# Optimization experiments

Hardware: AMD Instinct MI355X
Metric: run time of the kernel (lower is better)

Reference implementation:

```python
import jax, jax.numpy as jnp
import numpy as np

DIM = 768
NUM_HEADS = 12
HEAD_DIM = DIM // NUM_HEADS
SCALE = HEAD_DIM ** -0.5


def setup_inputs() -> dict:
    key = jax.random.key(0)
    k1, k2, k3, k4 = jax.random.split(key, 4)
    B, N = 4, 2048
    x = jax.random.normal(k1, (B, N, DIM), dtype=jnp.float32)
    w_qkv = jax.random.normal(k2, (DIM, 3 * DIM), dtype=jnp.float32) * (DIM ** -0.5)
    w_proj = jax.random.normal(k3, (DIM, DIM), dtype=jnp.float32) * (DIM ** -0.5)
    b_proj = jax.random.normal(k4, (DIM,), dtype=jnp.float32) * 0.02
    return {"x": x, "w_qkv": w_qkv, "w_proj": w_proj, "b_proj": b_proj}


def reference(x, w_qkv, w_proj, b_proj):
    B, N, C = x.shape
    H, Dh = NUM_HEADS, HEAD_DIM
    # qkv: [B, N, 3, H, Dh] -> q,k,v each [B, H, N, Dh]
    qkv = (x @ w_qkv).reshape(B, N, 3, H, Dh)
    q = qkv[:, :, 0].transpose(0, 2, 1, 3) * SCALE
    k = qkv[:, :, 1].transpose(0, 2, 1, 3)
    v = qkv[:, :, 2].transpose(0, 2, 1, 3)
    attn = jax.nn.softmax(jnp.einsum('bhnd,bhmd->bhnm', q, k), axis=-1)
    out = jnp.einsum('bhnm,bhmd->bhnd', attn, v)  # [B, H, N, Dh]
    out = out.transpose(0, 2, 1, 3).reshape(B, N, C)
    return out @ w_proj + b_proj
```

## Files before the change

kernel.cpp:

```cpp
#include <hip/hip_runtime.h>

typedef unsigned short u16;
typedef __bf16 bf16x8 __attribute__((ext_vector_type(8)));
typedef __bf16 bf16x4 __attribute__((ext_vector_type(4)));
typedef short s16x4 __attribute__((ext_vector_type(4)));
typedef float f32x4 __attribute__((ext_vector_type(4)));
typedef _Float16 f16x4 __attribute__((ext_vector_type(4)));
typedef unsigned short u16x8 __attribute__((ext_vector_type(8)));
typedef unsigned short u16x4 __attribute__((ext_vector_type(4)));

__device__ __forceinline__ u16 f2bf(float x) {
  union { float f; unsigned u; } c; c.f = x;
  unsigned r = c.u + 0x7FFFu + ((c.u >> 16) & 1u);
  return (u16)(r >> 16);
}

__device__ __forceinline__ void glds16(const void* g, void* s) {
  __builtin_amdgcn_global_load_lds(
      (const __attribute__((address_space(1))) unsigned int*)g,
      (__attribute__((address_space(3))) unsigned int*)s, 16, 0, 0);
}

__global__ __launch_bounds__(256) void k_pre(const float* __restrict__ x,
                                             u16* __restrict__ xbf,
                                             const float* __restrict__ wq,
                                             u16* __restrict__ wqt,
                                             const float* __restrict__ wp,
                                             u16* __restrict__ wpt) {
  __shared__ float tile[64 * 68];
  int bx = blockIdx.x;
  int tid = threadIdx.x;
  if (bx < 3072) {
    int i = bx * 256 + tid;
    const f32x4* xp = (const f32x4*)x + (size_t)i * 2;
    f32x4 a = xp[0], b = xp[1];
    u16x8 r;
    r[0] = f2bf(a[0]); r[1] = f2bf(a[1]); r[2] = f2bf(a[2]); r[3] = f2bf(a[3]);
    r[4] = f2bf(b[0]); r[5] = f2bf(b[1]); r[6] = f2bf(b[2]); r[7] = f2bf(b[3]);
    *((u16x8*)xbf + i) = r;
    return;
  }
  const float* src; u16* dst; int Nn, n0, k0;
  const int K = 768;
  if (bx < 3504) { int b2 = bx - 3072; src = wq; dst = wqt; Nn = 2304;
                   n0 = (b2 % 36) * 64; k0 = (b2 / 36) * 64; }
  else           { int b2 = bx - 3504; src = wp; dst = wpt; Nn = 768;
                   n0 = (b2 % 12) * 64; k0 = (b2 / 12) * 64; }
  int rr = tid >> 4, cc = tid & 15;
#pragma unroll
  for (int r = 0; r < 4; ++r) {
    int k = r * 16 + rr;
    f32x4 v = *(const f32x4*)(src + (size_t)(k0 + k) * Nn + n0 + cc * 4);
    *(f32x4*)(tile + k * 68 + cc * 4) = v;
  }
  __syncthreads();
#pragma unroll
  for (int r = 0; r < 4; ++r) {
    int n = r * 16 + rr;
    u16x4 o;
#pragma unroll
    for (int j = 0; j < 4; ++j) o[j] = f2bf(tile[(cc * 4 + j) * 68 + n]);
    *(u16x4*)(dst + (size_t)(n0 + n) * K + k0 + cc * 4) = o;
  }
}

template <int BM, int N, bool PROJ>
__global__ __launch_bounds__(256) void k_gemm(const u16* __restrict__ A,
                                              const u16* __restrict__ Bt,
                                              u16* __restrict__ Co,
                                              float* __restrict__ Cf,
                                              const float* __restrict__ bias,
                                              u16* __restrict__ vt) {
  const int K = 768;
  const int FI = BM / 32;
  __shared__ u16 lA[BM * 64];
  __shared__ u16 lB[128 * 64];
  const int tid = threadIdx.x;
  const int wave = tid >> 6, lane = tid & 63;
  const int lr = lane & 15, lq = lane >> 4;
  const int m0 = blockIdx.x * BM, n0 = blockIdx.y * 128;
  const int wr = (wave >> 1) * (BM / 2), wc = (wave & 1) * 64;
  f32x4 acc[FI][4] = {};
  for (int k0 = 0; k0 < K; k0 += 64) {
#pragma unroll
    for (int r = 0; r < BM / 32; ++r) {
      int ch = r * 256 + tid;
      int mm = ch >> 3, cs = ch & 7;
      glds16(A + (size_t)(m0 + mm) * K + k0 + ((cs ^ (mm & 7)) << 3), lA + ch * 8);
    }
#pragma unroll
    for (int r = 0; r < 4; ++r) {
      int ch = r * 256 + tid;
      int mm = ch >> 3, cs = ch & 7;
      glds16(Bt + (size_t)(n0 + mm) * K + k0 + ((cs ^ (mm & 7)) << 3), lB + ch * 8);
    }
    __syncthreads();
#pragma unroll
    for (int ks = 0; ks < 2; ++ks) {
      bf16x8 af[FI], bfr[4];
#pragma unroll
      for (int f = 0; f < FI; ++f) {
        int ma = wr + f * 16 + lr;
        af[f] = *(const bf16x8*)(lA + (ma * 8 + ((ks * 4 + lq) ^ (ma & 7))) * 8);
      }
#pragma unroll
      for (int f = 0; f < 4; ++f) {
        int nb = wc + f * 16 + lr;
        bfr[f] = *(const bf16x8*)(lB + (nb * 8 + ((ks * 4 + lq) ^ (nb & 7))) * 8);
      }
#pragma unroll
      for (int fi = 0; fi < FI; ++fi)
#pragma unroll
        for (int fj = 0; fj < 4; ++fj)
          acc[fi][fj] = __builtin_amdgcn_mfma_f32_16x16x32_bf16(
              af[fi], bfr[fj], acc[fi][fj], 0, 0, 0);
    }
    __syncthreads();
  }
#pragma unroll
  for (int fi = 0; fi < FI; ++fi) {
#pragma unroll
    for (int fj = 0; fj < 4; ++fj) {
      int row = m0 + wr + fi * 16 + lq * 4;
      int col = n0 + wc + fj * 16 + lr;
      if constexpr (PROJ) {
        float bv = bias[col];
#pragma unroll
        for (int g = 0; g < 4; ++g)
          Cf[(size_t)(row + g) * N + col] = acc[fi][fj][g] + bv;
      } else {
        if (n0 + wc >= 1536) {
          int hh = (col - 1536) >> 6, dd = col & 63;
          u16x4 o;
#pragma unroll
          for (int g = 0; g < 4; ++g) o[g] = f2bf(acc[fi][fj][g]);
          *(u16x4*)(vt + (((size_t)(row >> 11) * 12 + hh) * 64 + dd) * 2048 +
                    (row & 2047)) = o;
        } else {
          const float qs = 0.18033688011112042f;
          float s = (col < 768) ? qs : 1.0f;
#pragma unroll
          for (int g = 0; g < 4; ++g)
            Co[(size_t)(row + g) * N + col] = f2bf(acc[fi][fj][g] * s);
        }
      }
    }
  }
}

__global__ __launch_bounds__(256, 2) void k_attn(const u16* __restrict__ qkv,
                                                 const u16* __restrict__ vt,
                                                 u16* __restrict__ p0,
                                                 u16* __restrict__ p1,
                                                 float* __restrict__ Lp) {
  const int SEQ = 2048, C3 = 2304;
  __shared__ u16 lK[2][128 * 64];
  __shared__ u16 lV[2][64 * 128];
  const int tid = threadIdx.x;
  const int wave = tid >> 6, lane = tid & 63;
  const int lr = lane & 15, lq = lane >> 4;
  const int n0 = blockIdx.x * 128;
  const int bh = blockIdx.y;
  const int jh = blockIdx.z;
  const int b = bh / 12, h = bh % 12;
  const u16* qb = qkv + (size_t)b * SEQ * C3 + h * 64;
  const u16* kb = qb + 768;
  const u16* vb = vt + (size_t)bh * 64 * SEQ;

#pragma unroll
  for (int r = 0; r < 4; ++r) {
    int ch = r * 256 + tid;
    int mm = ch >> 3, cs = ch & 7;
    glds16(qb + (size_t)(n0 + mm) * C3 + ((cs ^ (mm & 7)) << 3), lK[0] + ch * 8);
  }
  __syncthreads();
  bf16x8 qf[2][2];
#pragma unroll
  for (int rf = 0; rf < 2; ++rf) {
    int mq = wave * 32 + rf * 16 + lr;
#pragma unroll
    for (int ks = 0; ks < 2; ++ks)
      qf[rf][ks] = *(const bf16x8*)(lK[0] + (mq * 8 + ((ks * 4 + lq) ^ (mq & 7))) * 8);
  }
  __syncthreads();

  const f32x4 biasC = {-8.f, -8.f, -8.f, -8.f};
  const s16x4 onesA = {16256, 16256, 16256, 16256};
  f32x4 O[2][4] = {};
  f32x4 L5[2] = {};

  const int smm = tid >> 3, scs = tid & 7;
  const int sdd = tid >> 4, sct = tid & 15;

  auto stage = [&](int t, int buf) {
    int j0 = jh * 1024 + t * 128;
#pragma unroll
    for (int r = 0; r < 4; ++r) {
      int ch = r * 256 + tid;
      int mm = (r << 5) + smm;
      glds16(kb + (size_t)(j0 + mm) * C3 + ((scs ^ (mm & 7)) << 3),
             lK[buf] + ch * 8);
      int dd = (r << 4) + sdd;
      glds16(vb + (size_t)dd * SEQ + j0 + ((sct ^ (dd & 7)) << 3),
             lV[buf] + ch * 8);
    }
  };

  stage(0, 0);
  for (int t = 0; t < 8; ++t) {
    const int cur = t & 1;
    const u16* K_ = lK[cur];
    const u16* V_ = lV[cur];
    asm volatile("s_barrier" ::: "memory");
    if (t < 7) {
      stage(t + 1, cur ^ 1);
      asm volatile("s_waitcnt vmcnt(8)" ::: "memory");
    } else {
      asm volatile("s_waitcnt vmcnt(0)" ::: "memory");
    }
    asm volatile("s_barrier" ::: "memory");

    f32x4 S[8][2];
#pragma unroll
    for (int cf = 0; cf < 8; ++cf) {
      int j = cf * 16 + lr;
      bf16x8 kf = *(const bf16x8*)(K_ + (j * 8 + (lq ^ (j & 7))) * 8);
#pragma unroll
      for (int rf = 0; rf < 2; ++rf)
        S[cf][rf] = __builtin_amdgcn_mfma_f32_16x16x32_bf16(
            kf, qf[rf][0], biasC, 0, 0, 0);
    }
#pragma unroll
    for (int cf = 0; cf < 8; ++cf) {
      int j = cf * 16 + lr;
      bf16x8 kf = *(const bf16x8*)(K_ + (j * 8 + ((4 + lq) ^ (j & 7))) * 8);
#pragma unroll
      for (int rf = 0; rf < 2; ++rf)
        S[cf][rf] = __builtin_amdgcn_mfma_f32_16x16x32_bf16(
            kf, qf[rf][1], S[cf][rf], 0, 0, 0);
    }
    union PU { bf16x4 b; s16x4 s; } P[8][2];
#pragma unroll
    for (int cf = 0; cf < 8; ++cf)
#pragma unroll
      for (int rf = 0; rf < 2; ++rf) {
        bf16x4 pb;
#pragma unroll
        for (int g = 0; g < 4; ++g)
          pb[g] = (__bf16)__builtin_amdgcn_exp2f(S[cf][rf][g]);
        P[cf][rf].b = pb;
      }
#pragma unroll
    for (int cf = 0; cf < 8; ++cf) {
      int c2 = cf * 2 + (lq >> 1);
#pragma unroll
      for (int rf = 0; rf < 2; ++rf)
        L5[rf] = __builtin_amdgcn_mfma_f32_16x16x16bf16_1k(
            onesA, P[cf][rf].s, L5[rf], 0, 0, 0);
#pragma unroll
      for (int df = 0; df < 4; ++df) {
        int d = df * 16 + lr;
        s16x4 vf = *(const s16x4*)(V_ + d * 128 + ((c2 ^ (d & 7)) << 3) + (lq & 1) * 4);
#pragma unroll
        for (int rf = 0; rf < 2; ++rf)
          O[rf][df] = __builtin_amdgcn_mfma_f32_16x16x16bf16_1k(
              vf, P[cf][rf].s, O[rf][df], 0, 0, 0);
      }
    }
  }

  u16* pd = jh ? p1 : p0;
  float* Lb = Lp + (size_t)(jh * 48 + bh) * 2048;
#pragma unroll
  for (int rf = 0; rf < 2; ++rf) {
    int rowl = n0 + wave * 32 + rf * 16 + lr;
    if (lq == 0) Lb[rowl] = L5[rf][0];
    size_t row = (size_t)b * SEQ + rowl;
#pragma unroll
    for (int df = 0; df < 4; ++df) {
      union { f16x4 h; u16x4 u; } o;
#pragma unroll
      for (int g = 0; g < 4; ++g) o.h[g] = (_Float16)O[rf][df][g];
      *(u16x4*)(pd + row * 768 + h * 64 + df * 16 + lq * 4) = o.u;
    }
  }
}

__global__ __launch_bounds__(256) void k_merge(const u16* __restrict__ p0,
                                               u16* __restrict__ p1,
                                               const float* __restrict__ Lp) {
  int t = blockIdx.x * 256 + threadIdx.x;
  int row = t / 192, c4 = (t % 192) * 4;
  int hh = c4 >> 6;
  int bh = (row >> 11) * 12 + hh, rowl = row & 2047;
  float l = Lp[(size_t)bh * 2048 + rowl] + Lp[(size_t)(48 + bh) * 2048 + rowl];
  float inv = 1.0f / l;
  size_t off = (size_t)row * 768 + c4;
  union { f16x4 h; u16x4 u; } a, bb;
  a.u = *(const u16x4*)(p0 + off);
  bb.u = *(const u16x4*)(p1 + off);
  u16x4 o;
#pragma unroll
  for (int g = 0; g < 4; ++g)
    o[g] = f2bf(((float)a.h[g] + (float)bb.h[g]) * inv);
  *(u16x4*)(p1 + off) = o;
}

extern "C" void kernel_launch(void* const* d_in, const int* in_sizes, int n_in,
                              void* d_out, int out_size, void* d_ws, size_t ws_size,
                              hipStream_t stream) {
  const float* x = (const float*)d_in[0];
  const float* w_qkv = (const float*)d_in[1];
  const float* w_proj = (const float*)d_in[2];
  const float* b_proj = (const float*)d_in[3];
  float* out = (float*)d_out;
  char* ws = (char*)d_ws;
  u16* x_bf    = (u16*)(ws);
  u16* wqkv_t  = (u16*)(ws + 12582912);
  u16* wproj_t = (u16*)(ws + 16121856);
  u16* qkv     = (u16*)(ws + 17301504);
  u16* vt      = (u16*)(ws + 55050240);
  u16* aout    = (u16*)(ws + 67633152);
  float* Lp    = (float*)wqkv_t;

  k_pre<<<3648, 256, 0, stream>>>(x, x_bf, w_qkv, wqkv_t, w_proj, wproj_t);
  k_gemm<128, 2304, false><<<dim3(64, 18), 256, 0, stream>>>(x_bf, wqkv_t, qkv,
                                                             nullptr, nullptr, vt);
  k_attn<<<dim3(16, 48, 2), 256, 0, stream>>>(qkv, vt, x_bf, aout, Lp);
  k_merge<<<6144, 256, 0, stream>>>(x_bf, aout, Lp);
  k_gemm<64, 768, true><<<dim3(128, 6), 256, 0, stream>>>(aout, wproj_t, nullptr,
                                                          out, b_proj, nullptr);
}
```

Baseline: 233.6 us.

## Widen attention query tile to 256 rows and use 16x16x32 MFMA for PV

Each attention block now handles 256 query rows (64 per wave) instead of 128, so every K/V tile staged into LDS is reused across twice as many queries and the grid shrinks by half. The PV product and the row-sum now use the 16x16x32 bf16 MFMA on 8-element P fragments rather than the 16x16x16 variant. To support this, the QKV GEMM writes V-transposed with a permuted sequence order so that each lane's 8-element V read lines up with the S fragment layout. This raises register pressure (4x4 accumulators plus 4x2 Q fragments) and halves the block count, which may hurt occupancy and load balance.

```diff
diff --git a/kernel.cpp b/kernel.cpp
--- a/kernel.cpp
+++ b/kernel.cpp
@@ -2,8 +2,6 @@
 
 typedef unsigned short u16;
 typedef __bf16 bf16x8 __attribute__((ext_vector_type(8)));
-typedef __bf16 bf16x4 __attribute__((ext_vector_type(4)));
-typedef short s16x4 __attribute__((ext_vector_type(4)));
 typedef float f32x4 __attribute__((ext_vector_type(4)));
 typedef _Float16 f16x4 __attribute__((ext_vector_type(4)));
 typedef unsigned short u16x8 __attribute__((ext_vector_type(8)));
@@ -131,11 +129,15 @@
       } else {
         if (n0 + wc >= 1536) {
           int hh = (col - 1536) >> 6, dd = col & 63;
+          int sl = row & 2047;
+          int g4 = (sl >> 2) & 31;
+          int p = ((g4 >> 3) << 3) | ((g4 & 3) << 1) | ((g4 >> 2) & 1);
+          int seqp = (sl & ~127) | (p << 2);
           u16x4 o;
 #pragma unroll
           for (int g = 0; g < 4; ++g) o[g] = f2bf(acc[fi][fj][g]);
           *(u16x4*)(vt + (((size_t)(row >> 11) * 12 + hh) * 64 + dd) * 2048 +
-                    (row & 2047)) = o;
+                    seqp) = o;
         } else {
           const float qs = 0.18033688011112042f;
           float s = (col < 768) ? qs : 1.0f;
@@ -154,12 +156,11 @@
                                                  u16* __restrict__ p1,
                                                  float* __restrict__ Lp) {
   const int SEQ = 2048, C3 = 2304;
-  __shared__ u16 lK[2][128 * 64];
-  __shared__ u16 lV[2][64 * 128];
+  __shared__ u16 lds[32768];
   const int tid = threadIdx.x;
   const int wave = tid >> 6, lane = tid & 63;
   const int lr = lane & 15, lq = lane >> 4;
-  const int n0 = blockIdx.x * 128;
+  const int n0 = blockIdx.x * 256;
   const int bh = blockIdx.y;
   const int jh = blockIdx.z;
   const int b = bh / 12, h = bh % 12;
@@ -168,49 +169,53 @@
   const u16* vb = vt + (size_t)bh * 64 * SEQ;
 
 #pragma unroll
-  for (int r = 0; r < 4; ++r) {
+  for (int r = 0; r < 8; ++r) {
     int ch = r * 256 + tid;
     int mm = ch >> 3, cs = ch & 7;
-    glds16(qb + (size_t)(n0 + mm) * C3 + ((cs ^ (mm & 7)) << 3), lK[0] + ch * 8);
+    glds16(qb + (size_t)(n0 + mm) * C3 + ((cs ^ (mm & 7)) << 3), lds + ch * 8);
   }
   __syncthreads();
-  bf16x8 qf[2][2];
-#pragma unroll
-  for (int rf = 0; rf < 2; ++rf) {
-    int mq = wave * 32 + rf * 16 + lr;
+  bf16x8 qf[4][2];
+#pragma unroll
+  for (int rf = 0; rf < 4; ++rf) {
+    int mq = wave * 64 + rf * 16 + lr;
 #pragma unroll
     for (int ks = 0; ks < 2; ++ks)
-      qf[rf][ks] = *(const bf16x8*)(lK[0] + (mq * 8 + ((ks * 4 + lq) ^ (mq & 7))) * 8);
+      qf[rf][ks] = *(const bf16x8*)(lds + (mq * 8 + ((ks * 4 + lq) ^ (mq & 7))) * 8);
   }
   __syncthreads();
 
   const f32x4 biasC = {-8.f, -8.f, -8.f, -8.f};
-  const s16x4 onesA = {16256, 16256, 16256, 16256};
-  f32x4 O[2][4] = {};
-  f32x4 L5[2] = {};
-
-  const int smm = tid >> 3, scs = tid & 7;
-  const int sdd = tid >> 4, sct = tid & 15;
+  union { u16x8 u; bf16x8 b; } onesU;
+#pragma unroll
+  for (int e = 0; e < 8; ++e) onesU.u[e] = 0x3F80;
+  const bf16x8 onesA = onesU.b;
+  f32x4 O[4][4] = {};
+  f32x4 L5[4] = {};
 
   auto stage = [&](int t, int buf) {
     int j0 = jh * 1024 + t * 128;
+    u16* K_ = lds + buf * 8192;
+    u16* V_ = lds + 16384 + buf * 8192;
 #pragma unroll
     for (int r = 0; r < 4; ++r) {
       int ch = r * 256 + tid;
-      int mm = (r << 5) + smm;
-      glds16(kb + (size_t)(j0 + mm) * C3 + ((scs ^ (mm & 7)) << 3),
-             lK[buf] + ch * 8);
-      int dd = (r << 4) + sdd;
-      glds16(vb + (size_t)dd * SEQ + j0 + ((sct ^ (dd & 7)) << 3),
-             lV[buf] + ch * 8);
+      int mm = ch >> 3, cs = ch & 7;
+      glds16(kb + (size_t)(j0 + mm) * C3 + ((cs ^ (mm & 7)) << 3), K_ + ch * 8);
+    }
+#pragma unroll
+    for (int r = 0; r < 4; ++r) {
+      int ch = r * 256 + tid;
+      int dd = ch >> 4, ct = ch & 15;
+      glds16(vb + (size_t)dd * SEQ + j0 + ((ct ^ (dd & 7)) << 3), V_ + ch * 8);
     }
   };
 
   stage(0, 0);
   for (int t = 0; t < 8; ++t) {
     const int cur = t & 1;
-    const u16* K_ = lK[cur];
-    const u16* V_ = lV[cur];
+    const u16* K_ = lds + cur * 8192;
+    const u16* V_ = lds + 16384 + cur * 8192;
     asm volatile("s_barrier" ::: "memory");
     if (t < 7) {
       stage(t + 1, cur ^ 1);
@@ -220,51 +225,48 @@
     }
     asm volatile("s_barrier" ::: "memory");
 
-    f32x4 S[8][2];
-#pragma unroll
-    for (int cf = 0; cf < 8; ++cf) {
-      int j = cf * 16 + lr;
-      bf16x8 kf = *(const bf16x8*)(K_ + (j * 8 + (lq ^ (j & 7))) * 8);
-#pragma unroll
-      for (int rf = 0; rf < 2; ++rf)
-        S[cf][rf] = __builtin_amdgcn_mfma_f32_16x16x32_bf16(
-            kf, qf[rf][0], biasC, 0, 0, 0);
-    }
-#pragma unroll
-    for (int cf = 0; cf < 8; ++cf) {
-      int j = cf * 16 + lr;
-      bf16x8 kf = *(const bf16x8*)(K_ + (j * 8 + ((4 + lq) ^ (j & 7))) * 8);
-#pragma unroll
-      for (int rf = 0; rf < 2; ++rf)
-        S[cf][rf] = __builtin_amdgcn_mfma_f32_16x16x32_bf16(
-            kf, qf[rf][1], S[cf][rf], 0, 0, 0);
-    }
-    union PU { bf16x4 b; s16x4 s; } P[8][2];
-#pragma unroll
-    for (int cf = 0; cf < 8; ++cf)
-#pragma unroll
-      for (int rf = 0; rf < 2; ++rf) {
-        bf16x4 pb;
-#pragma unroll
-        for (int g = 0; g < 4; ++g)
-          pb[g] = (__bf16)__builtin_amdgcn_exp2f(S[cf][rf][g]);
-        P[cf][rf].b = pb;
-      }
-#pragma unroll
-    for (int cf = 0; cf < 8; ++cf) {
-      int c2 = cf * 2 + (lq >> 1);
-#pragma unroll
-      for (int rf = 0; rf < 2; ++rf)
-        L5[rf] = __builtin_amdgcn_mfma_f32_16x16x16bf16_1k(
-            onesA, P[cf][rf].s, L5[rf], 0, 0, 0);
+#pragma unroll
+    for (int c = 0; c < 4; ++c) {
+      f32x4 S[2][4];
+#pragma unroll
+      for (int j2 = 0; j2 < 2; ++j2) {
+        int j = (c * 2 + j2) * 16 + lr;
+        bf16x8 kf = *(const bf16x8*)(K_ + (j * 8 + (lq ^ (j & 7))) * 8);
+#pragma unroll
+        for (int rf = 0; rf < 4; ++rf)
+          S[j2][rf] = __builtin_amdgcn_mfma_f32_16x16x32_bf16(
+              kf, qf[rf][0], biasC, 0, 0, 0);
+      }
+#pragma unroll
+      for (int j2 = 0; j2 < 2; ++j2) {
+        int j = (c * 2 + j2) * 16 + lr;
+        bf16x8 kf = *(const bf16x8*)(K_ + (j * 8 + ((4 + lq) ^ (j & 7))) * 8);
+#pragma unroll
+        for (int rf = 0; rf < 4; ++rf)
+          S[j2][rf] = __builtin_amdgcn_mfma_f32_16x16x32_bf16(
+              kf, qf[rf][1], S[j2][rf], 0, 0, 0);
+      }
+      bf16x8 P[4];
+#pragma unroll
+      for (int rf = 0; rf < 4; ++rf) {
+        bf16x8 p8;
+#pragma unroll
+        for (int j2 = 0; j2 < 2; ++j2)
+#pragma unroll
+          for (int g = 0; g < 4; ++g)
+            p8[j2 * 4 + g] = (__bf16)__builtin_amdgcn_exp2f(S[j2][rf][g]);
+        P[rf] = p8;
+        L5[rf] = __builtin_amdgcn_mfma_f32_16x16x32_bf16(
+            onesA, P[rf], L5[rf], 0, 0, 0);
+      }
 #pragma unroll
       for (int df = 0; df < 4; ++df) {
         int d = df * 16 + lr;
-        s16x4 vf = *(const s16x4*)(V_ + d * 128 + ((c2 ^ (d & 7)) << 3) + (lq & 1) * 4);
-#pragma unroll
-        for (int rf = 0; rf < 2; ++rf)
-          O[rf][df] = __builtin_amdgcn_mfma_f32_16x16x16bf16_1k(
-              vf, P[cf][rf].s, O[rf][df], 0, 0, 0);
+        bf16x8 vf = *(const bf16x8*)(V_ + d * 128 + (((c * 4 + lq) ^ (d & 7)) << 3));
+#pragma unroll
+        for (int rf = 0; rf < 4; ++rf)
+          O[rf][df] = __builtin_amdgcn_mfma_f32_16x16x32_bf16(
+              vf, P[rf], O[rf][df], 0, 0, 0);
       }
     }
   }
@@ -272,8 +274,8 @@
   u16* pd = jh ? p1 : p0;
   float* Lb = Lp + (size_t)(jh * 48 + bh) * 2048;
 #pragma unroll
-  for (int rf = 0; rf < 2; ++rf) {
-    int rowl = n0 + wave * 32 + rf * 16 + lr;
+  for (int rf = 0; rf < 4; ++rf) {
+    int rowl = n0 + wave * 64 + rf * 16 + lr;
     if (lq == 0) Lb[rowl] = L5[rf][0];
     size_t row = (size_t)b * SEQ + rowl;
 #pragma unroll
@@ -326,7 +328,7 @@
   k_pre<<<3648, 256, 0, stream>>>(x, x_bf, w_qkv, wqkv_t, w_proj, wproj_t);
   k_gemm<128, 2304, false><<<dim3(64, 18), 256, 0, stream>>>(x_bf, wqkv_t, qkv,
                                                              nullptr, nullptr, vt);
-  k_attn<<<dim3(16, 48, 2), 256, 0, stream>>>(qkv, vt, x_bf, aout, Lp);
+  k_attn<<<dim3(8, 48, 2), 256, 0, stream>>>(qkv, vt, x_bf, aout, Lp);
   k_merge<<<6144, 256, 0, stream>>>(x_bf, aout, Lp);
   k_gemm<64, 768, true><<<dim3(128, 6), 256, 0, stream>>>(aout, wproj_t, nullptr,
                                                           out, b_proj, nullptr);
```

New measurement: 215.9 us. 1.08x faster.
